# Performance work log

Hardware: AMD Instinct MI355X
Metric: run time of the kernel (lower is better)

## Reference

```python
import jax, jax.numpy as jnp
import numpy as np


def phi(x):
    # ELU + 1 feature map (Katharopoulos et al. 2020)
    return jax.nn.elu(x) + 1.0


def setup_inputs() -> dict:
    key = jax.random.key(0)
    k1, k2, k3 = jax.random.split(key, 3)
    B, T, D = 2, 2048, 512
    x = jax.random.normal(k1, (B, T, D), dtype=jnp.float32)
    # torch nn.Linear stores weight as (out_features, in_features)
    w_qkv = jax.random.normal(k2, (3 * D, D), dtype=jnp.float32) * 0.02
    w_out = jax.random.normal(k3, (D, D), dtype=jnp.float32) * 0.02
    return {"x": x, "w_qkv": w_qkv, "w_out": w_out, "n_heads": 16}


def reference(x, w_qkv, w_out, n_heads):
    B, T, D = x.shape
    H = n_heads
    Dh = D // H
    qkv = x @ w_qkv.T                                   # (B,T,3D)
    qkv = qkv.reshape(B, T, 3, H, Dh).transpose(2, 0, 3, 1, 4)  # (3,B,H,T,Dh)
    q, k, v = phi(qkv[0]), phi(qkv[1]), qkv[2]
    # kv outer product: (B,H,T,Dh_k,Dh_v), causal cumsum over time
    kv = k[..., :, None] * v[..., None, :]
    kv_cumsum = jnp.cumsum(kv, axis=2)
    num = jnp.einsum('bhtd,bhtde->bhte', q, kv_cumsum)  # (B,H,T,Dh)
    k_cumsum = jnp.cumsum(k, axis=2)
    denom = jnp.einsum('bhtd,bhtd->bht', q, k_cumsum)[..., None]
    denom = jnp.maximum(denom, 1e-6)
    out = num / denom                                   # (B,H,T,Dh)
    out = out.transpose(0, 2, 1, 3).reshape(B, T, D)
    return out @ w_out.T
```

## Files before the change

### kernel.cpp

```cpp
#include <hip/hip_runtime.h>
#include <hip/hip_bf16.h>
#include <math.h>

#define B_ 2
#define T_ 2048
#define D_ 512
#define H_ 16
#define DH 32
#define L_ 64
#define C_ 32
#define NC 1024
#define VTP 72
#define CSZ 1056

typedef __attribute__((ext_vector_type(8))) short bf16x8;
typedef __attribute__((ext_vector_type(4))) float f32x4;
typedef __attribute__((ext_vector_type(4))) unsigned short u16x4;

#define AS1 __attribute__((address_space(1)))
#define AS3 __attribute__((address_space(3)))

__device__ __forceinline__ float bf2f(unsigned short u) {
    union { float f; unsigned int i; } v; v.i = ((unsigned int)u) << 16; return v.f;
}
__device__ __forceinline__ unsigned short f2bf(float f) {
    union { float f; unsigned int u; } v; v.f = f;
    unsigned int u = v.u;
    unsigned int r = u + 0x7FFFu + ((u >> 16) & 1u);
    return (unsigned short)(r >> 16);
}
__device__ __forceinline__ unsigned short f2bf_rne(float f) {
    __hip_bfloat16 h = __float2bfloat16(f);
    union { __hip_bfloat16 h; unsigned short u; } v; v.h = h; return v.u;
}
__device__ __forceinline__ bf16x8 phi_frag(bf16x8 in) {
    bf16x8 r;
    #pragma unroll
    for (int i = 0; i < 8; ++i) {
        float f = bf2f((unsigned short)in[i]);
        f = f > 0.f ? f + 1.f : __expf(f);
        r[i] = (short)f2bf(f);
    }
    return r;
}
__device__ __forceinline__ void gload_lds16(const unsigned short* g, unsigned short* l) {
    __builtin_amdgcn_global_load_lds((const AS1 unsigned int*)g, (AS3 unsigned int*)l, 16, 0, 0);
}

template<int BM, bool AF32, bool OUT_BF16>
__global__ __launch_bounds__(256) void gemm_nt(const void* __restrict__ Aptr,
                                               const float* __restrict__ Wf,
                                               void* __restrict__ Cout,
                                               int N, int K)
{
    constexpr int MF = BM / 32;
    constexpr int AF4 = BM / 32;
    __shared__ unsigned short As[2][BM][32];
    __shared__ unsigned short Bs[2][128][32];
    const int tid = threadIdx.x;
    const int lane = tid & 63;
    const int wave = tid >> 6;
    const int wr = wave >> 1;
    const int wc = wave & 1;
    const size_t bm = (size_t)blockIdx.x * BM;
    const size_t bn = (size_t)blockIdx.y * 128;

    const int r8 = lane >> 3;
    const int c4 = (lane & 7) * 4;
    const int lrow = lane >> 2;
    const int lcol = (lane & 3) * 8;

    const float* agf = nullptr;
    const unsigned short* agb = nullptr;
    if constexpr (AF32) agf = (const float*)Aptr + (bm + wave * (BM / 4) + r8) * (size_t)K + c4;
    else                agb = (const unsigned short*)Aptr + (bm + wave * (BM / 4) + lrow) * (size_t)K + lcol;
    const float* wgf = Wf + (bn + wave * 32 + r8) * (size_t)K + c4;

    f32x4 aL[AF4];
    f32x4 wL[4];

    auto load_stage = [&](int buf, int k0) {
        if constexpr (AF32) {
            #pragma unroll
            for (int i = 0; i < AF4; ++i)
                aL[i] = *(const f32x4*)(agf + k0 + (size_t)(i * 8) * K);
        } else {
            gload_lds16(agb + k0, &As[buf][wave * (BM / 4)][0]);
            if constexpr (BM / 4 == 32)
                gload_lds16(agb + (size_t)16 * K + k0, &As[buf][wave * (BM / 4) + 16][0]);
        }
        #pragma unroll
        for (int i = 0; i < 4; ++i)
            wL[i] = *(const f32x4*)(wgf + k0 + (size_t)(i * 8) * K);
    };
    auto write_stage = [&](int buf) {
        if constexpr (AF32) {
            #pragma unroll
            for (int i = 0; i < AF4; ++i) {
                u16x4 o;
                o.x = f2bf_rne(aL[i][0]); o.y = f2bf_rne(aL[i][1]);
                o.z = f2bf_rne(aL[i][2]); o.w = f2bf_rne(aL[i][3]);
                *(u16x4*)&As[buf][wave * (BM / 4) + r8 + i * 8][c4] = o;
            }
        }
        #pragma unroll
        for (int i = 0; i < 4; ++i) {
            u16x4 o;
            o.x = f2bf_rne(wL[i][0]); o.y = f2bf_rne(wL[i][1]);
            o.z = f2bf_rne(wL[i][2]); o.w = f2bf_rne(wL[i][3]);
            *(u16x4*)&Bs[buf][wave * 32 + r8 + i * 8][c4] = o;
        }
    };

    f32x4 acc[MF][4];
    #pragma unroll
    for (int m = 0; m < MF; ++m)
        #pragma unroll
        for (int n = 0; n < 4; ++n)
            acc[m][n] = (f32x4){0.f, 0.f, 0.f, 0.f};

    const int rr = lane & 15;
    const int kb = (lane >> 4) * 8;

    load_stage(0, 0);
    write_stage(0);
    __syncthreads();
    int cur = 0;
    for (int k0 = 0; k0 < K; k0 += 32) {
        const bool more = k0 + 32 < K;
        if (more) load_stage(cur ^ 1, k0 + 32);
        bf16x8 af[MF], bfr[4];
        #pragma unroll
        for (int m = 0; m < MF; ++m)
            af[m] = *(const bf16x8*)&As[cur][wr * (BM / 2) + m * 16 + rr][kb];
        #pragma unroll
        for (int n = 0; n < 4; ++n)
            bfr[n] = *(const bf16x8*)&Bs[cur][wc * 64 + n * 16 + rr][kb];
        #pragma unroll
        for (int m = 0; m < MF; ++m)
            #pragma unroll
            for (int n = 0; n < 4; ++n)
                acc[m][n] = __builtin_amdgcn_mfma_f32_16x16x32_bf16(af[m], bfr[n], acc[m][n], 0, 0, 0);
        if (more) write_stage(cur ^ 1);
        __syncthreads();
        cur ^= 1;
    }

    const int cr = (lane >> 4) * 4;
    const int cc = lane & 15;
    #pragma unroll
    for (int m = 0; m < MF; ++m)
        #pragma unroll
        for (int n = 0; n < 4; ++n)
            #pragma unroll
            for (int j = 0; j < 4; ++j) {
                size_t row = bm + wr * (BM / 2) + m * 16 + cr + j;
                size_t col = bn + wc * 64 + n * 16 + cc;
                float v = acc[m][n][j];
                if (OUT_BF16) ((unsigned short*)Cout)[row * N + col] = f2bf(v);
                else          ((float*)Cout)[row * N + col] = v;
            }
}

__global__ __launch_bounds__(256) void chunk_sum(const unsigned short* __restrict__ qkv,
                                                 float* __restrict__ cSf)
{
    __shared__ unsigned short Kt[4][DH][VTP];
    __shared__ unsigned short Vt[4][48][VTP];
    const int tid = threadIdx.x;
    const int lane = tid & 63;
    const int wave = tid >> 6;
    const int chunk = blockIdx.x * 4 + wave;
    const int c = chunk & 31;
    const int h = (chunk >> 5) & 15;
    const int b = chunk >> 9;
    const size_t rowbase = ((size_t)(b * T_ + c * L_)) * (3 * D_) + h * DH;
    const int half = lane & 1;

    #pragma unroll
    for (int it = 0; it < 2; ++it) {
        int t = (lane >> 1) + it * 32;
        const unsigned short* kp = qkv + rowbase + (size_t)t * (3 * D_) + D_ + half * 16;
        const unsigned short* vp = qkv + rowbase + (size_t)t * (3 * D_) + 2 * D_ + half * 16;
        bf16x8 k0 = phi_frag(*(const bf16x8*)kp);
        bf16x8 k1 = phi_frag(*(const bf16x8*)(kp + 8));
        bf16x8 v0 = *(const bf16x8*)vp;
        bf16x8 v1 = *(const bf16x8*)(vp + 8);
        #pragma unroll
        for (int i = 0; i < 8; ++i) {
            Kt[wave][half * 16 + i][t]     = (unsigned short)k0[i];
            Kt[wave][half * 16 + 8 + i][t] = (unsigned short)k1[i];
            Vt[wave][half * 16 + i][t]     = (unsigned short)v0[i];
            Vt[wave][half * 16 + 8 + i][t] = (unsigned short)v1[i];
        }
    }
    Vt[wave][32][lane] = 0x3F80;

    const int fr = lane & 15;
    const int fg = lane >> 4;
    f32x4 acc[3][2];
    #pragma unroll
    for (int m = 0; m < 3; ++m)
        #pragma unroll
        for (int n = 0; n < 2; ++n)
            acc[m][n] = (f32x4){0.f, 0.f, 0.f, 0.f};

    #pragma unroll
    for (int ks = 0; ks < 2; ++ks) {
        int toff = fg * 8 + ks * 32;
        bf16x8 av[3], bk[2];
        #pragma unroll
        for (int m = 0; m < 3; ++m) av[m] = *(const bf16x8*)&Vt[wave][m * 16 + fr][toff];
        #pragma unroll
        for (int n = 0; n < 2; ++n) bk[n] = *(const bf16x8*)&Kt[wave][n * 16 + fr][toff];
        #pragma unroll
        for (int m = 0; m < 3; ++m)
            #pragma unroll
            for (int n = 0; n < 2; ++n)
                acc[m][n] = __builtin_amdgcn_mfma_f32_16x16x32_bf16(av[m], bk[n], acc[m][n], 0, 0, 0);
    }

    float* outp = cSf + (size_t)chunk * CSZ;
    #pragma unroll
    for (int m = 0; m < 2; ++m)
        #pragma unroll
        for (int n = 0; n < 2; ++n)
            #pragma unroll
            for (int r = 0; r < 4; ++r)
                outp[(m * 16 + fg * 4 + r) * 32 + n * 16 + fr] = acc[m][n][r];
    if (fg == 0) {
        #pragma unroll
        for (int n = 0; n < 2; ++n)
            outp[32 * 32 + n * 16 + fr] = acc[2][n][0];
    }
}

__global__ __launch_bounds__(256) void chunk_scan(const float* __restrict__ cSf,
                                                  unsigned short* __restrict__ cSt)
{
    int idx = blockIdx.x * 256 + threadIdx.x;
    int bh = idx / CSZ;
    int r  = idx % CSZ;
    const float* src = cSf + (size_t)bh * C_ * CSZ + r;
    unsigned short* dst = cSt + (size_t)bh * C_ * CSZ + r;
    float v[C_];
    #pragma unroll
    for (int c = 0; c < C_; ++c) v[c] = src[(size_t)c * CSZ];
    float acc = 0.f;
    #pragma unroll
    for (int c = 0; c < C_; ++c) {
        dst[(size_t)c * CSZ] = f2bf(acc);
        acc += v[c];
    }
}

__global__ __launch_bounds__(256) void chunk_out(const unsigned short* __restrict__ qkv,
                                                 const unsigned short* __restrict__ cSt,
                                                 unsigned short* __restrict__ attn)
{
    __shared__ unsigned short Vt[48][VTP];
    __shared__ unsigned short Am[4][16][VTP];
    const int tid = threadIdx.x;
    const int lane = tid & 63;
    const int w = tid >> 6;
    const int chunk = blockIdx.x;
    const int c = chunk & 31;
    const int h = (chunk >> 5) & 15;
    const int b = chunk >> 9;
    const size_t rowbase = ((size_t)(b * T_ + c * L_)) * (3 * D_) + h * DH;
    const int fr = lane & 15;
    const int fg = lane >> 4;

    {
        int t = w * 16 + (lane >> 2);
        int q = lane & 3;
        const unsigned short* vp = qkv + rowbase + (size_t)t * (3 * D_) + 2 * D_ + q * 8;
        bf16x8 v0 = *(const bf16x8*)vp;
        #pragma unroll
        for (int i = 0; i < 8; ++i)
            Vt[q * 8 + i][t] = (unsigned short)v0[i];
        if (q == 0) Vt[32][t] = 0x3F80;
    }

    bf16x8 aq;
    {
        const unsigned short* qp = qkv + rowbase + (size_t)(w * 16 + fr) * (3 * D_) + fg * 8;
        aq = phi_frag(*(const bf16x8*)qp);
    }
    bf16x8 bk[4];
    #pragma unroll
    for (int n = 0; n < 4; ++n) {
        if (n <= w) {
            const unsigned short* kp = qkv + rowbase + (size_t)(n * 16 + fr) * (3 * D_) + D_ + fg * 8;
            bk[n] = phi_frag(*(const bf16x8*)kp);
        }
    }
    bf16x8 bkv[3];
    #pragma unroll
    for (int n = 0; n < 3; ++n)
        bkv[n] = *(const bf16x8*)&cSt[(size_t)chunk * CSZ + (size_t)(n * 16 + fr) * 32 + fg * 8];

    f32x4 zero = (f32x4){0.f, 0.f, 0.f, 0.f};
    f32x4 acc[3];
    #pragma unroll
    for (int n = 0; n < 3; ++n)
        acc[n] = __builtin_amdgcn_mfma_f32_16x16x32_bf16(aq, bkv[n], zero, 0, 0, 0);

    #pragma unroll
    for (int n = 0; n < 4; ++n) {
        if (n <= w) {
            f32x4 s = __builtin_amdgcn_mfma_f32_16x16x32_bf16(aq, bk[n], zero, 0, 0, 0);
            #pragma unroll
            for (int r = 0; r < 4; ++r) {
                unsigned short v = f2bf(s[r]);
                if (n == w && fr > fg * 4 + r) v = 0;
                Am[w][fg * 4 + r][n * 16 + fr] = v;
            }
        }
    }
    if ((w & 1) == 0) {
        int zc = (w + 1) * 16;
        *(uint2*)&Am[w][lane >> 2][zc + (lane & 3) * 4] = (uint2){0u, 0u};
    }
    __syncthreads();

    #pragma unroll
    for (int ks = 0; ks < 2; ++ks) {
        if (ks <= (w >> 1)) {
            bf16x8 bv[3];
            #pragma unroll
            for (int n = 0; n < 3; ++n)
                bv[n] = *(const bf16x8*)&Vt[n * 16 + fr][fg * 8 + ks * 32];
            bf16x8 aa = *(const bf16x8*)&Am[w][fr][fg * 8 + ks * 32];
            #pragma unroll
            for (int n = 0; n < 3; ++n)
                acc[n] = __builtin_amdgcn_mfma_f32_16x16x32_bf16(aa, bv[n], acc[n], 0, 0, 0);
        }
    }

    float dn[4];
    #pragma unroll
    for (int r = 0; r < 4; ++r)
        dn[r] = __shfl(acc[2][r], lane & 48);
    #pragma unroll
    for (int r = 0; r < 4; ++r) {
        float inv = 1.0f / fmaxf(dn[r], 1e-6f);
        #pragma unroll
        for (int n = 0; n < 2; ++n)
            Am[w][fg * 4 + r][n * 16 + fr] = f2bf(acc[n][r] * inv);
    }
    {
        int lrow = lane >> 2;
        int q = lane & 3;
        uint4 o = *(const uint4*)&Am[w][lrow][q * 8];
        size_t grow = (size_t)(b * T_ + c * L_ + w * 16 + lrow);
        *(uint4*)(attn + grow * D_ + h * DH + q * 8) = o;
    }
}

extern "C" void kernel_launch(void* const* d_in, const int* in_sizes, int n_in,
                              void* d_out, int out_size, void* d_ws, size_t ws_size,
                              hipStream_t stream) {
    const float* x     = (const float*)d_in[0];
    const float* w_qkv = (const float*)d_in[1];
    const float* w_out = (const float*)d_in[2];
    float* out = (float*)d_out;

    char* ws = (char*)d_ws;
    unsigned short* qkvb  = (unsigned short*)ws;
    unsigned short* attnb = (unsigned short*)(ws + 12582912);
    float* cSf            = (float*)(ws + 16777216);
    unsigned short* cSt   = (unsigned short*)(ws + 21102592);

    gemm_nt<64, true, true><<<dim3(4096 / 64, 1536 / 128), 256, 0, stream>>>(
        x, w_qkv, qkvb, 1536, 512);

    chunk_sum<<<NC / 4, 256, 0, stream>>>(qkvb, cSf);

    chunk_scan<<<132, 256, 0, stream>>>(cSf, cSt);

    chunk_out<<<NC, 256, 0, stream>>>(qkvb, cSt, attnb);

    gemm_nt<64, false, false><<<dim3(4096 / 64, 512 / 128), 256, 0, stream>>>(
        attnb, w_out, out, 512, 512);
}
```

Measured before the change: 49.03 us.

## Fuse QKV projection GEMM with per-chunk KV state summation

```diff
diff --git a/kernel.cpp b/kernel.cpp
--- a/kernel.cpp
+++ b/kernel.cpp
@@ -33,18 +33,160 @@
     __hip_bfloat16 h = __float2bfloat16(f);
     union { __hip_bfloat16 h; unsigned short u; } v; v.h = h; return v.u;
 }
+__device__ __forceinline__ float phi_s(float f) {
+    return f > 0.f ? f + 1.f : __expf(f);
+}
 __device__ __forceinline__ bf16x8 phi_frag(bf16x8 in) {
     bf16x8 r;
     #pragma unroll
     for (int i = 0; i < 8; ++i) {
         float f = bf2f((unsigned short)in[i]);
-        f = f > 0.f ? f + 1.f : __expf(f);
-        r[i] = (short)f2bf(f);
+        r[i] = (short)f2bf(phi_s(f));
     }
     return r;
 }
 __device__ __forceinline__ void gload_lds16(const unsigned short* g, unsigned short* l) {
     __builtin_amdgcn_global_load_lds((const AS1 unsigned int*)g, (AS3 unsigned int*)l, 16, 0, 0);
+}
+
+struct __align__(16) ShQ {
+    union {
+        struct { unsigned short As[2][64][32]; unsigned short Bs[2][96][32]; } g;
+        struct { unsigned short Kt[DH][VTP]; unsigned short Vt[48][VTP]; } s;
+    };
+};
+
+__global__ __launch_bounds__(256) void gemm_qkv_cs(const float* __restrict__ x,
+                                                   const float* __restrict__ W,
+                                                   unsigned short* __restrict__ qkvb,
+                                                   float* __restrict__ cSf)
+{
+    __shared__ ShQ sh;
+    const int tid = threadIdx.x;
+    const int lane = tid & 63;
+    const int w = tid >> 6;
+    const int chunk = blockIdx.x;
+    const int c = chunk & 31;
+    const int h = (chunk >> 5) & 15;
+    const int b = chunk >> 9;
+    const size_t R0 = (size_t)(b * T_ + c * L_);
+
+    const int sr = tid >> 3;
+    const int sc = (tid & 7) * 4;
+    const float* ax  = x + (R0 + sr) * 512 + sc;
+    const float* wgq = W + ((size_t)(h * DH) + sr) * 512 + sc;
+    const float* wgk = W + ((size_t)(D_ + h * DH) + sr) * 512 + sc;
+    const float* wgv = W + ((size_t)(2 * D_ + h * DH) + sr) * 512 + sc;
+
+    f32x4 aL[2], wL[3];
+    auto load_stage = [&](int k0) {
+        aL[0] = *(const f32x4*)(ax + k0);
+        aL[1] = *(const f32x4*)(ax + k0 + (size_t)32 * 512);
+        wL[0] = *(const f32x4*)(wgq + k0);
+        wL[1] = *(const f32x4*)(wgk + k0);
+        wL[2] = *(const f32x4*)(wgv + k0);
+    };
+    auto cvt4 = [](f32x4 v) {
+        u16x4 o;
+        o.x = f2bf_rne(v[0]); o.y = f2bf_rne(v[1]);
+        o.z = f2bf_rne(v[2]); o.w = f2bf_rne(v[3]);
+        return o;
+    };
+    auto write_stage = [&](int buf) {
+        *(u16x4*)&sh.g.As[buf][sr][sc]      = cvt4(aL[0]);
+        *(u16x4*)&sh.g.As[buf][sr + 32][sc] = cvt4(aL[1]);
+        *(u16x4*)&sh.g.Bs[buf][sr][sc]      = cvt4(wL[0]);
+        *(u16x4*)&sh.g.Bs[buf][sr + 32][sc] = cvt4(wL[1]);
+        *(u16x4*)&sh.g.Bs[buf][sr + 64][sc] = cvt4(wL[2]);
+    };
+
+    f32x4 acc[6];
+    #pragma unroll
+    for (int n = 0; n < 6; ++n) acc[n] = (f32x4){0.f, 0.f, 0.f, 0.f};
+
+    const int rr = lane & 15;
+    const int fg = lane >> 4;
+    const int kb = fg * 8;
+
+    load_stage(0);
+    write_stage(0);
+    __syncthreads();
+    int cur = 0;
+    for (int k0 = 0; k0 < 512; k0 += 32) {
+        const bool more = k0 + 32 < 512;
+        if (more) load_stage(k0 + 32);
+        bf16x8 af = *(const bf16x8*)&sh.g.As[cur][w * 16 + rr][kb];
+        bf16x8 bfr[6];
+        #pragma unroll
+        for (int n = 0; n < 6; ++n)
+            bfr[n] = *(const bf16x8*)&sh.g.Bs[cur][n * 16 + rr][kb];
+        #pragma unroll
+        for (int n = 0; n < 6; ++n)
+            acc[n] = __builtin_amdgcn_mfma_f32_16x16x32_bf16(af, bfr[n], acc[n], 0, 0, 0);
+        if (more) write_stage(cur ^ 1);
+        __syncthreads();
+        cur ^= 1;
+    }
+
+    {
+        const int colbase[6] = { h * DH, h * DH + 16,
+                                 D_ + h * DH, D_ + h * DH + 16,
+                                 2 * D_ + h * DH, 2 * D_ + h * DH + 16 };
+        #pragma unroll
+        for (int n = 0; n < 6; ++n)
+            #pragma unroll
+            for (int j = 0; j < 4; ++j) {
+                size_t row = R0 + w * 16 + fg * 4 + j;
+                qkvb[row * 1536 + colbase[n] + rr] = f2bf(acc[n][j]);
+            }
+    }
+
+    #pragma unroll
+    for (int n = 2; n < 4; ++n)
+        #pragma unroll
+        for (int j = 0; j < 4; ++j)
+            sh.s.Kt[(n - 2) * 16 + rr][w * 16 + fg * 4 + j] = f2bf(phi_s(acc[n][j]));
+    #pragma unroll
+    for (int n = 4; n < 6; ++n)
+        #pragma unroll
+        for (int j = 0; j < 4; ++j)
+            sh.s.Vt[(n - 4) * 16 + rr][w * 16 + fg * 4 + j] = f2bf(acc[n][j]);
+    if (rr == 0) {
+        #pragma unroll
+        for (int j = 0; j < 4; ++j)
+            sh.s.Vt[32][w * 16 + fg * 4 + j] = 0x3F80;
+    }
+    __syncthreads();
+
+    if (w < 3) {
+        f32x4 a2[2];
+        a2[0] = (f32x4){0.f, 0.f, 0.f, 0.f};
+        a2[1] = (f32x4){0.f, 0.f, 0.f, 0.f};
+        #pragma unroll
+        for (int ks = 0; ks < 2; ++ks) {
+            int toff = fg * 8 + ks * 32;
+            bf16x8 av = *(const bf16x8*)&sh.s.Vt[w * 16 + rr][toff];
+            bf16x8 bkk[2];
+            #pragma unroll
+            for (int n = 0; n < 2; ++n)
+                bkk[n] = *(const bf16x8*)&sh.s.Kt[n * 16 + rr][toff];
+            #pragma unroll
+            for (int n = 0; n < 2; ++n)
+                a2[n] = __builtin_amdgcn_mfma_f32_16x16x32_bf16(av, bkk[n], a2[n], 0, 0, 0);
+        }
+        float* outp = cSf + (size_t)chunk * CSZ;
+        if (w < 2) {
+            #pragma unroll
+            for (int n = 0; n < 2; ++n)
+                #pragma unroll
+                for (int r = 0; r < 4; ++r)
+                    outp[(w * 16 + fg * 4 + r) * 32 + n * 16 + rr] = a2[n][r];
+        } else if (fg == 0) {
+            #pragma unroll
+            for (int n = 0; n < 2; ++n)
+                outp[32 * 32 + n * 16 + rr] = a2[n][0];
+        }
+    }
 }
 
 template<int BM, bool AF32, bool OUT_BF16>
@@ -162,79 +304,6 @@
             }
 }
 
-__global__ __launch_bounds__(256) void chunk_sum(const unsigned short* __restrict__ qkv,
-                                                 float* __restrict__ cSf)
-{
-    __shared__ unsigned short Kt[4][DH][VTP];
-    __shared__ unsigned short Vt[4][48][VTP];
-    const int tid = threadIdx.x;
-    const int lane = tid & 63;
-    const int wave = tid >> 6;
-    const int chunk = blockIdx.x * 4 + wave;
-    const int c = chunk & 31;
-    const int h = (chunk >> 5) & 15;
-    const int b = chunk >> 9;
-    const size_t rowbase = ((size_t)(b * T_ + c * L_)) * (3 * D_) + h * DH;
-    const int half = lane & 1;
-
-    #pragma unroll
-    for (int it = 0; it < 2; ++it) {
-        int t = (lane >> 1) + it * 32;
-        const unsigned short* kp = qkv + rowbase + (size_t)t * (3 * D_) + D_ + half * 16;
-        const unsigned short* vp = qkv + rowbase + (size_t)t * (3 * D_) + 2 * D_ + half * 16;
-        bf16x8 k0 = phi_frag(*(const bf16x8*)kp);
-        bf16x8 k1 = phi_frag(*(const bf16x8*)(kp + 8));
-        bf16x8 v0 = *(const bf16x8*)vp;
-        bf16x8 v1 = *(const bf16x8*)(vp + 8);
-        #pragma unroll
-        for (int i = 0; i < 8; ++i) {
-            Kt[wave][half * 16 + i][t]     = (unsigned short)k0[i];
-            Kt[wave][half * 16 + 8 + i][t] = (unsigned short)k1[i];
-            Vt[wave][half * 16 + i][t]     = (unsigned short)v0[i];
-            Vt[wave][half * 16 + 8 + i][t] = (unsigned short)v1[i];
-        }
-    }
-    Vt[wave][32][lane] = 0x3F80;
-
-    const int fr = lane & 15;
-    const int fg = lane >> 4;
-    f32x4 acc[3][2];
-    #pragma unroll
-    for (int m = 0; m < 3; ++m)
-        #pragma unroll
-        for (int n = 0; n < 2; ++n)
-            acc[m][n] = (f32x4){0.f, 0.f, 0.f, 0.f};
-
-    #pragma unroll
-    for (int ks = 0; ks < 2; ++ks) {
-        int toff = fg * 8 + ks * 32;
-        bf16x8 av[3], bk[2];
-        #pragma unroll
-        for (int m = 0; m < 3; ++m) av[m] = *(const bf16x8*)&Vt[wave][m * 16 + fr][toff];
-        #pragma unroll
-        for (int n = 0; n < 2; ++n) bk[n] = *(const bf16x8*)&Kt[wave][n * 16 + fr][toff];
-        #pragma unroll
-        for (int m = 0; m < 3; ++m)
-            #pragma unroll
-            for (int n = 0; n < 2; ++n)
-                acc[m][n] = __builtin_amdgcn_mfma_f32_16x16x32_bf16(av[m], bk[n], acc[m][n], 0, 0, 0);
-    }
-
-    float* outp = cSf + (size_t)chunk * CSZ;
-    #pragma unroll
-    for (int m = 0; m < 2; ++m)
-        #pragma unroll
-        for (int n = 0; n < 2; ++n)
-            #pragma unroll
-            for (int r = 0; r < 4; ++r)
-                outp[(m * 16 + fg * 4 + r) * 32 + n * 16 + fr] = acc[m][n][r];
-    if (fg == 0) {
-        #pragma unroll
-        for (int n = 0; n < 2; ++n)
-            outp[32 * 32 + n * 16 + fr] = acc[2][n][0];
-    }
-}
-
 __global__ __launch_bounds__(256) void chunk_scan(const float* __restrict__ cSf,
                                                   unsigned short* __restrict__ cSt)
 {
@@ -372,10 +441,7 @@
     float* cSf            = (float*)(ws + 16777216);
     unsigned short* cSt   = (unsigned short*)(ws + 21102592);
 
-    gemm_nt<64, true, true><<<dim3(4096 / 64, 1536 / 128), 256, 0, stream>>>(
-        x, w_qkv, qkvb, 1536, 512);
-
-    chunk_sum<<<NC / 4, 256, 0, stream>>>(qkvb, cSf);
+    gemm_qkv_cs<<<NC, 256, 0, stream>>>(x, w_qkv, qkvb, cSf);
 
     chunk_scan<<<132, 256, 0, stream>>>(cSf, cSt);
 
```

Result: faster. 47.57 us (-3.0%).
